# Optimization experiments

Measured on AMD Instinct MI355X. Metric: run time of the kernel, lower is better.

Reference implementation:

```python
import jax, jax.numpy as jnp
import numpy as np

N = 200000
D = 256          # d_node
H = 1024         # n_hidden
OUT = 4002       # n_out
L = 2001
G = 4096         # number of graphs (static)


def _linear_params(key, fan_in, fan_out):
    kw, kb = jax.random.split(key)
    s = 1.0 / np.sqrt(fan_in)
    W = jax.random.uniform(kw, (fan_in, fan_out), jnp.float32, -s, s)
    b = jax.random.uniform(kb, (fan_out,), jnp.float32, -s, s)
    return W, b


def setup_inputs() -> dict:
    key = jax.random.key(0)
    ks = jax.random.split(key, 6)
    h = jax.random.normal(ks[0], (N, D), dtype=jnp.float32)
    node_graph_index = jnp.sort(jax.random.randint(ks[1], (N,), 0, G, dtype=jnp.int32))
    W_pool, b_pool = _linear_params(ks[2], D, D)
    W1, b1 = _linear_params(ks[3], D, H)
    W2, b2 = _linear_params(ks[4], H, H)
    W3, b3 = _linear_params(ks[5], H, OUT)
    return {"h": h, "node_graph_index": node_graph_index,
            "W_pool": W_pool, "b_pool": b_pool,
            "W1": W1, "b1": b1, "W2": W2, "b2": b2, "W3": W3, "b3": b3}


def reference(h, node_graph_index, W_pool, b_pool, W1, b1, W2, b2, W3, b3):
    # attention logits per node: SiLU(W_pool h + b)   [N, D]
    att = jax.nn.silu(h @ W_pool + b_pool)
    # per-graph, per-feature softmax over nodes (segment softmax)
    att_max = jax.ops.segment_max(att, node_graph_index, num_segments=G)   # [G, D]
    att_exp = jnp.exp(att - att_max[node_graph_index])                     # [N, D]
    att_sum = jax.ops.segment_sum(att_exp, node_graph_index, num_segments=G)  # [G, D]
    att_norm = att_exp / jnp.maximum(att_sum[node_graph_index], 1e-12)     # [N, D]
    # attention-weighted pooling
    h_G = jax.ops.segment_sum(h * att_norm, node_graph_index, num_segments=G)  # [G, D]
    # output MLP (depth=2 hidden SiLU layers, plain last)
    x = jax.nn.silu(h_G @ W1 + b1)
    x = jax.nn.silu(x @ W2 + b2)
    out = x @ W3 + b3                                                      # [G, 4002]
    eps_imag = out[:, :L]
    eps_real = out[:, L:]
    return out, eps_imag, eps_real
```

## Files before the change

### kernel.cpp

```cpp
#include <hip/hip_runtime.h>
#include <cstdint>
#include <cstddef>

#define NN 200000
#define DD 256
#define HH 1024
#define OUTD 4002
#define LL 2001
#define GG 4096

#define ROWS_PB 128
#define STEPS 8
#define SLOTS_L 8
#define SLOTS_G 4

typedef unsigned short u16;
typedef short short8 __attribute__((ext_vector_type(8)));
typedef float f32x4 __attribute__((ext_vector_type(4)));

static __device__ __forceinline__ u16 f2bf(float f) {
  uint32_t u = __float_as_uint(f);
  uint32_t r = (u + 0x7FFFu + ((u >> 16) & 1u)) >> 16;
  return (u16)r;
}
static __device__ __forceinline__ float bf2f(u16 b) {
  return __uint_as_float(((uint32_t)b) << 16);
}

static __device__ __forceinline__ void gld_lds16(const void* g, void* l) {
  __builtin_amdgcn_global_load_lds((const __attribute__((address_space(1))) void*)g,
                                   (__attribute__((address_space(3))) void*)l,
                                   16, 0, 0);
}

static __device__ __forceinline__ void barrier_nodrain() {
  asm volatile("s_waitcnt lgkmcnt(0)" ::: "memory");
  __builtin_amdgcn_s_barrier();
  __builtin_amdgcn_sched_barrier(0);
}

__global__ __launch_bounds__(256) void transpose_bf16(const float* __restrict__ W,
                                                      u16* __restrict__ WT,
                                                      int K, int Nc) {
  __shared__ float tile[32][33];
  int nt = blockIdx.x * 32, kt = blockIdx.y * 32;
  int tx = threadIdx.x & 31, ty = threadIdx.x >> 5;
#pragma unroll
  for (int i = 0; i < 4; ++i) {
    int k = kt + ty + i * 8, n = nt + tx;
    tile[ty + i * 8][tx] = (k < K && n < Nc) ? W[(size_t)k * Nc + n] : 0.f;
  }
  __syncthreads();
#pragma unroll
  for (int i = 0; i < 4; ++i) {
    int n = nt + ty + i * 8, k = kt + tx;
    if (n < Nc && k < K) WT[(size_t)n * K + k] = f2bf(tile[tx][ty + i * 8]);
  }
}

__global__ void graph_offsets(const int* __restrict__ idx, int* __restrict__ offs) {
  int g = blockIdx.x * blockDim.x + threadIdx.x;
  if (g > GG) return;
  int lo = 0, hi = NN;
  while (lo < hi) {
    int mid = (lo + hi) >> 1;
    if (idx[mid] < g) lo = mid + 1; else hi = mid;
  }
  offs[g] = lo;
}

__global__ __launch_bounds__(512) void fused_pool(const float* __restrict__ h,
                                                  const u16* __restrict__ WT,
                                                  const float* __restrict__ bias,
                                                  const int* __restrict__ idx,
                                                  const int* __restrict__ offs,
                                                  float* __restrict__ PS_ss,
                                                  float* __restrict__ PS_ah) {
  __shared__ __align__(16) u16 At[2][16 * 256];
  __shared__ float accS[SLOTS_L * 256];
  __shared__ float accA[SLOTS_L * 256];
  __shared__ int lidx[ROWS_PB];

  const int tid = threadIdx.x;
  const int wave = tid >> 6, lane = tid & 63;
  const int rl = lane & 15, q = lane >> 4;
  const int b = blockIdx.x;
  const long row0 = (long)b * ROWS_PB;

  if (tid < ROWS_PB) {
    long r = row0 + tid;
    lidx[tid] = (r < NN) ? idx[r] : -1;
  }
  for (int i = tid; i < SLOTS_L * 256; i += 512) { accS[i] = 0.f; accA[i] = 0.f; }

  const int f0 = wave * 32 + rl, f1 = f0 + 16;
  short8 Bf0[8], Bf1[8];
  {
    const u16* wp0 = WT + (size_t)f0 * 256 + q * 8;
    const u16* wp1 = WT + (size_t)f1 * 256 + q * 8;
#pragma unroll
    for (int k0 = 0; k0 < 8; ++k0) {
      Bf0[k0] = *reinterpret_cast<const short8*>(wp0 + k0 * 32);
      Bf1[k0] = *reinterpret_cast<const short8*>(wp1 + k0 * 32);
    }
  }
  const float bv0 = bias[f0], bv1 = bias[f1];

  const int tr = tid >> 5, te = (tid & 31) * 8;
  const int wbyte = tr * 512 + ((te * 2) ^ ((tr & 7) << 4));
  float4 pf0, pf1;
  auto issue = [&](int st) {
    long r = row0 + (long)st * 16 + tr;
    if (r >= NN) r = NN - 1;
    const float* p = h + r * 256 + te;
    pf0 = *reinterpret_cast<const float4*>(p);
    pf1 = *reinterpret_cast<const float4*>(p + 4);
  };
  auto commit = [&](int bufsel) {
    short8 w;
    w[0] = (short)f2bf(pf0.x); w[1] = (short)f2bf(pf0.y);
    w[2] = (short)f2bf(pf0.z); w[3] = (short)f2bf(pf0.w);
    w[4] = (short)f2bf(pf1.x); w[5] = (short)f2bf(pf1.y);
    w[6] = (short)f2bf(pf1.z); w[7] = (short)f2bf(pf1.w);
    *reinterpret_cast<short8*>((char*)&At[0][0] + bufsel * 8192 + wbyte) = w;
  };

  int afoff[8], hv0off[4], hv1off[4];
#pragma unroll
  for (int k0 = 0; k0 < 8; ++k0)
    afoff[k0] = rl * 512 + ((k0 * 64 + q * 16) ^ ((rl & 7) << 4));
#pragma unroll
  for (int reg = 0; reg < 4; ++reg) {
    int rloc = q * 4 + reg;
    hv0off[reg] = rloc * 512 + ((f0 * 2) ^ ((rloc & 7) << 4));
    hv1off[reg] = rloc * 512 + ((f1 * 2) ^ ((rloc & 7) << 4));
  }

  issue(0);
  commit(0);
  issue(1);
  barrier_nodrain();

  const int gfirst = lidx[0];
  int cur = -1;
  float ss0 = 0.f, ss1 = 0.f, ah0 = 0.f, ah1 = 0.f;

#pragma unroll
  for (int st = 0; st < STEPS; ++st) {
    const char* Ab = (const char*)&At[0][0] + (st & 1) * 8192;
    short8 af[8];
#pragma unroll
    for (int k0 = 0; k0 < 8; ++k0)
      af[k0] = *reinterpret_cast<const short8*>(Ab + afoff[k0]);
    f32x4 acc0 = {0.f, 0.f, 0.f, 0.f}, acc1 = {0.f, 0.f, 0.f, 0.f};
#pragma unroll
    for (int k0 = 0; k0 < 8; ++k0) {
      acc0 = __builtin_amdgcn_mfma_f32_16x16x32_bf16(af[k0], Bf0[k0], acc0, 0, 0, 0);
      acc1 = __builtin_amdgcn_mfma_f32_16x16x32_bf16(af[k0], Bf1[k0], acc1, 0, 0, 0);
    }
#pragma unroll
    for (int reg = 0; reg < 4; ++reg) {
      const int rloc = q * 4 + reg;
      const int gid = lidx[st * 16 + rloc];
      float z0 = acc0[reg] + bv0, z1 = acc1[reg] + bv1;
      float a0 = z0 / (1.f + __expf(-z0));
      float a1 = z1 / (1.f + __expf(-z1));
      float x0 = __expf(a0), x1 = __expf(a1);
      float hv0 = bf2f(*reinterpret_cast<const u16*>(Ab + hv0off[reg]));
      float hv1 = bf2f(*reinterpret_cast<const u16*>(Ab + hv1off[reg]));
      if (gid != cur) {
        if (cur >= 0) {
          int sl = cur - gfirst; if (sl >= SLOTS_L) sl = SLOTS_L - 1;
          atomicAdd(&accS[sl * 256 + f0], ss0);
          atomicAdd(&accA[sl * 256 + f0], ah0);
          atomicAdd(&accS[sl * 256 + f1], ss1);
          atomicAdd(&accA[sl * 256 + f1], ah1);
        }
        ss0 = ss1 = ah0 = ah1 = 0.f;
        cur = gid;
      }
      if (gid >= 0) {
        ss0 += x0; ah0 = __builtin_fmaf(x0, hv0, ah0);
        ss1 += x1; ah1 = __builtin_fmaf(x1, hv1, ah1);
      }
    }
    if (st + 1 < STEPS) {
      commit((st + 1) & 1);
      if (st + 2 < STEPS) issue(st + 2);
    }
    barrier_nodrain();
  }

  if (cur >= 0) {
    int sl = cur - gfirst; if (sl >= SLOTS_L) sl = SLOTS_L - 1;
    atomicAdd(&accS[sl * 256 + f0], ss0);
    atomicAdd(&accA[sl * 256 + f0], ah0);
    atomicAdd(&accS[sl * 256 + f1], ss1);
    atomicAdd(&accA[sl * 256 + f1], ah1);
  }
  __syncthreads();

  long lastrow = row0 + ROWS_PB - 1; if (lastrow >= NN) lastrow = NN - 1;
  const int glast = idx[lastrow];
  int gspan = glast - gfirst + 1; if (gspan > SLOTS_L) gspan = SLOTS_L;
  const int f = tid & 255, which = tid >> 8;
  for (int s = 0; s < gspan; ++s) {
    int g = gfirst + s;
    int osl = b - (offs[g] >> 7);
    if (osl < 0) osl = 0;
    if (osl >= SLOTS_G) osl = SLOTS_G - 1;
    float v = which ? accA[s * 256 + f] : accS[s * 256 + f];
    float* dst = which ? PS_ah : PS_ss;
    dst[((size_t)g * SLOTS_G + osl) * 256 + f] = v;
  }
}

__global__ __launch_bounds__(256) void finalize_pool(const float* __restrict__ PS_ss,
                                                     const float* __restrict__ PS_ah,
                                                     const int* __restrict__ offs,
                                                     u16* __restrict__ hG) {
  int i = blockIdx.x * 256 + threadIdx.x;
  int g = i >> 8, f = i & 255;
  int s0 = offs[g], s1 = offs[g + 1];
  float o = 0.f;
  if (s1 > s0) {
    int b0 = s0 >> 7, b1 = (s1 - 1) >> 7;
    int nsl = b1 - b0 + 1; if (nsl > SLOTS_G) nsl = SLOTS_G;
    float ss = 0.f, ah = 0.f;
    for (int s = 0; s < nsl; ++s) {
      ss += PS_ss[((size_t)g * SLOTS_G + s) * 256 + f];
      ah += PS_ah[((size_t)g * SLOTS_G + s) * 256 + f];
    }
    o = ah / fmaxf(ss, 1e-12f);
  }
  hG[i] = f2bf(o);
}

template <int SILU, int MODE, int BK>
__global__ __launch_bounds__(512) void gemm_bt(const u16* __restrict__ A,
                                               const u16* __restrict__ BT,
                                               const float* __restrict__ bias,
                                               u16* __restrict__ Cb,
                                               float* __restrict__ Cf,
                                               float* __restrict__ Ci,
                                               float* __restrict__ Cr,
                                               int M, int Nn, int K) {
  constexpr int NSUB = BK / 32;
  __shared__ __align__(16) u16 As[2][NSUB][128 * 32];
  __shared__ __align__(16) u16 Bs[2][NSUB][128 * 32];
  const int tid = threadIdx.x;
  const int wave = tid >> 6, lane = tid & 63;
  const int wr = wave >> 2, wc = wave & 3;
  const long bm = (long)blockIdx.y * 128;
  const long bn = (long)blockIdx.x * 128;

  const f32x4 zero = {0.f, 0.f, 0.f, 0.f};
  f32x4 acc[4][2];
#pragma unroll
  for (int i = 0; i < 4; ++i)
#pragma unroll
    for (int j = 0; j < 2; ++j) acc[i][j] = zero;

  const int rg = lane >> 2;
  const int kc = (lane & 3) * 8;
  const int rl = lane & 15;
  const int kk = (lane >> 4) * 8;
  const int rbase = wave * 16;
  const int nt = K / BK;

  auto stage = [&](int t, int buf) {
    const long k0 = (long)t * BK;
#pragma unroll
    for (int s = 0; s < NSUB; ++s) {
      long rA = bm + rbase + rg; if (rA >= M) rA = M - 1;
      long rB = bn + rbase + rg; if (rB >= Nn) rB = Nn - 1;
      gld_lds16(A + rA * K + k0 + s * 32 + kc, &As[buf][s][rbase * 32]);
      gld_lds16(BT + rB * K + k0 + s * 32 + kc, &Bs[buf][s][rbase * 32]);
    }
  };

  stage(0, 0);
  for (int t = 0; t < nt; ++t) {
    const int buf = t & 1;
    if (t + 1 < nt) {
      stage(t + 1, buf ^ 1);
      if constexpr (NSUB == 1) {
        asm volatile("s_waitcnt vmcnt(2)" ::: "memory");
      } else {
        asm volatile("s_waitcnt vmcnt(4)" ::: "memory");
      }
    } else {
      asm volatile("s_waitcnt vmcnt(0)" ::: "memory");
    }
    __builtin_amdgcn_s_barrier();
    __builtin_amdgcn_sched_barrier(0);

#pragma unroll
    for (int s = 0; s < NSUB; ++s) {
      short8 af[4], bfr[2];
#pragma unroll
      for (int mi = 0; mi < 4; ++mi)
        af[mi] = *reinterpret_cast<const short8*>(&As[buf][s][(wr * 64 + mi * 16 + rl) * 32 + kk]);
#pragma unroll
      for (int ni = 0; ni < 2; ++ni)
        bfr[ni] = *reinterpret_cast<const short8*>(&Bs[buf][s][(wc * 32 + ni * 16 + rl) * 32 + kk]);
#pragma unroll
      for (int mi = 0; mi < 4; ++mi)
#pragma unroll
        for (int ni = 0; ni < 2; ++ni)
          acc[mi][ni] = __builtin_amdgcn_mfma_f32_16x16x32_bf16(af[mi], bfr[ni], acc[mi][ni], 0, 0, 0);
    }

    asm volatile("s_waitcnt lgkmcnt(0)" ::: "memory");
    __builtin_amdgcn_s_barrier();
    __builtin_amdgcn_sched_barrier(0);
  }

#pragma unroll
  for (int ni = 0; ni < 2; ++ni) {
    long ccol = bn + wc * 32 + ni * 16 + rl;
    if (ccol >= Nn) continue;
    float bv = bias[ccol];
#pragma unroll
    for (int mi = 0; mi < 4; ++mi) {
#pragma unroll
      for (int reg = 0; reg < 4; ++reg) {
        long rrow = bm + wr * 64 + mi * 16 + (lane >> 4) * 4 + reg;
        if (rrow >= M) continue;
        float v = acc[mi][ni][reg] + bv;
        if (SILU) v = v / (1.f + __expf(-v));
        if (MODE == 0) {
          Cb[rrow * Nn + ccol] = f2bf(v);
        } else {
          Cf[rrow * (long)OUTD + ccol] = v;
          if (ccol < LL) Ci[rrow * (long)LL + ccol] = v;
          else           Cr[rrow * (long)LL + (ccol - LL)] = v;
        }
      }
    }
  }
}

extern "C" void kernel_launch(void* const* d_in, const int* in_sizes, int n_in,
                              void* d_out, int out_size, void* d_ws, size_t ws_size,
                              hipStream_t stream) {
  const float* h      = (const float*)d_in[0];
  const int*   idx    = (const int*)d_in[1];
  const float* W_pool = (const float*)d_in[2];
  const float* b_pool = (const float*)d_in[3];
  const float* W1     = (const float*)d_in[4];
  const float* b1     = (const float*)d_in[5];
  const float* W2     = (const float*)d_in[6];
  const float* b2     = (const float*)d_in[7];
  const float* W3     = (const float*)d_in[8];
  const float* b3     = (const float*)d_in[9];

  float* out   = (float*)d_out;
  float* out_i = out + (size_t)GG * OUTD;
  float* out_r = out_i + (size_t)GG * LL;

  char* ws = (char*)d_ws;
  size_t off = 0;
  auto alloc = [&](size_t bytes) {
    void* p = ws + off;
    off += (bytes + 255) & ~(size_t)255;
    return p;
  };
  u16* WpoolT = (u16*)alloc((size_t)DD * DD * 2);
  u16* W1T    = (u16*)alloc((size_t)HH * DD * 2);
  u16* W2T    = (u16*)alloc((size_t)HH * HH * 2);
  u16* W3T    = (u16*)alloc((size_t)OUTD * HH * 2);
  u16* hG     = (u16*)alloc((size_t)GG * DD * 2);
  u16* x1     = (u16*)alloc((size_t)GG * HH * 2);
  u16* x2     = (u16*)alloc((size_t)GG * HH * 2);
  int* offs   = (int*)alloc((GG + 1) * sizeof(int));
  float* PS_ss = (float*)alloc((size_t)GG * SLOTS_G * 256 * 4);
  float* PS_ah = (float*)alloc((size_t)GG * SLOTS_G * 256 * 4);

  transpose_bf16<<<dim3(8, 8), 256, 0, stream>>>(W_pool, WpoolT, DD, DD);
  transpose_bf16<<<dim3(32, 8), 256, 0, stream>>>(W1, W1T, DD, HH);
  transpose_bf16<<<dim3(32, 32), 256, 0, stream>>>(W2, W2T, HH, HH);
  transpose_bf16<<<dim3(126, 32), 256, 0, stream>>>(W3, W3T, HH, OUTD);
  graph_offsets<<<(GG + 256) / 256, 256, 0, stream>>>(idx, offs);

  fused_pool<<<(NN + ROWS_PB - 1) / ROWS_PB, 512, 0, stream>>>(
      h, WpoolT, b_pool, idx, offs, PS_ss, PS_ah);
  finalize_pool<<<GG, 256, 0, stream>>>(PS_ss, PS_ah, offs, hG);

  gemm_bt<1, 0, 64><<<dim3(8, 32), 512, 0, stream>>>(
      hG, W1T, b1, x1, nullptr, nullptr, nullptr, GG, HH, DD);
  gemm_bt<1, 0, 64><<<dim3(8, 32), 512, 0, stream>>>(
      x1, W2T, b2, x2, nullptr, nullptr, nullptr, GG, HH, HH);
  gemm_bt<0, 1, 32><<<dim3(32, 32), 512, 0, stream>>>(
      x2, W3T, b3, nullptr, out, out_i, out_r, GG, OUTD, HH);
}
```

Before: 287.0 us.

## Split pooling kernel across two feature halves per row chunk

The fused pooling kernel now launches a 2D grid in which each block handles 128 of the 256 output features for its 128-row chunk, instead of all 256. Each wave computes one MFMA output tile instead of two, which halves per-thread registers and LDS accumulators and doubles the number of blocks, aiming at higher occupancy and parallelism. In exchange, every h row chunk is loaded and converted to bf16 twice, once by each half-block, which doubles global reads of the largest input and the conversion work.

```diff
diff --git a/kernel.cpp b/kernel.cpp
--- a/kernel.cpp
+++ b/kernel.cpp
@@ -77,34 +77,34 @@
                                                   float* __restrict__ PS_ss,
                                                   float* __restrict__ PS_ah) {
   __shared__ __align__(16) u16 At[2][16 * 256];
-  __shared__ float accS[SLOTS_L * 256];
-  __shared__ float accA[SLOTS_L * 256];
+  __shared__ float accS[SLOTS_L * 128];
+  __shared__ float accA[SLOTS_L * 128];
   __shared__ int lidx[ROWS_PB];
 
   const int tid = threadIdx.x;
   const int wave = tid >> 6, lane = tid & 63;
   const int rl = lane & 15, q = lane >> 4;
-  const int b = blockIdx.x;
-  const long row0 = (long)b * ROWS_PB;
+  const int half = blockIdx.x;
+  const int chunk = blockIdx.y;
+  const int halfbase = half * 128;
+  const long row0 = (long)chunk * ROWS_PB;
 
   if (tid < ROWS_PB) {
     long r = row0 + tid;
     lidx[tid] = (r < NN) ? idx[r] : -1;
   }
-  for (int i = tid; i < SLOTS_L * 256; i += 512) { accS[i] = 0.f; accA[i] = 0.f; }
-
-  const int f0 = wave * 32 + rl, f1 = f0 + 16;
-  short8 Bf0[8], Bf1[8];
+  for (int i = tid; i < SLOTS_L * 128; i += 512) { accS[i] = 0.f; accA[i] = 0.f; }
+
+  const int fl = wave * 16 + rl;
+  const int f0 = halfbase + fl;
+  short8 Bf0[8];
   {
     const u16* wp0 = WT + (size_t)f0 * 256 + q * 8;
-    const u16* wp1 = WT + (size_t)f1 * 256 + q * 8;
-#pragma unroll
-    for (int k0 = 0; k0 < 8; ++k0) {
+#pragma unroll
+    for (int k0 = 0; k0 < 8; ++k0)
       Bf0[k0] = *reinterpret_cast<const short8*>(wp0 + k0 * 32);
-      Bf1[k0] = *reinterpret_cast<const short8*>(wp1 + k0 * 32);
-    }
-  }
-  const float bv0 = bias[f0], bv1 = bias[f1];
+  }
+  const float bv0 = bias[f0];
 
   const int tr = tid >> 5, te = (tid & 31) * 8;
   const int wbyte = tr * 512 + ((te * 2) ^ ((tr & 7) << 4));
@@ -125,7 +125,7 @@
     *reinterpret_cast<short8*>((char*)&At[0][0] + bufsel * 8192 + wbyte) = w;
   };
 
-  int afoff[8], hv0off[4], hv1off[4];
+  int afoff[8], hv0off[4];
 #pragma unroll
   for (int k0 = 0; k0 < 8; ++k0)
     afoff[k0] = rl * 512 + ((k0 * 64 + q * 16) ^ ((rl & 7) << 4));
@@ -133,7 +133,6 @@
   for (int reg = 0; reg < 4; ++reg) {
     int rloc = q * 4 + reg;
     hv0off[reg] = rloc * 512 + ((f0 * 2) ^ ((rloc & 7) << 4));
-    hv1off[reg] = rloc * 512 + ((f1 * 2) ^ ((rloc & 7) << 4));
   }
 
   issue(0);
@@ -143,7 +142,7 @@
 
   const int gfirst = lidx[0];
   int cur = -1;
-  float ss0 = 0.f, ss1 = 0.f, ah0 = 0.f, ah1 = 0.f;
+  float ss0 = 0.f, ah0 = 0.f;
 
 #pragma unroll
   for (int st = 0; st < STEPS; ++st) {
@@ -152,36 +151,30 @@
 #pragma unroll
     for (int k0 = 0; k0 < 8; ++k0)
       af[k0] = *reinterpret_cast<const short8*>(Ab + afoff[k0]);
-    f32x4 acc0 = {0.f, 0.f, 0.f, 0.f}, acc1 = {0.f, 0.f, 0.f, 0.f};
-#pragma unroll
-    for (int k0 = 0; k0 < 8; ++k0) {
+    f32x4 acc0 = {0.f, 0.f, 0.f, 0.f};
+#pragma unroll
+    for (int k0 = 0; k0 < 8; ++k0)
       acc0 = __builtin_amdgcn_mfma_f32_16x16x32_bf16(af[k0], Bf0[k0], acc0, 0, 0, 0);
-      acc1 = __builtin_amdgcn_mfma_f32_16x16x32_bf16(af[k0], Bf1[k0], acc1, 0, 0, 0);
-    }
 #pragma unroll
     for (int reg = 0; reg < 4; ++reg) {
       const int rloc = q * 4 + reg;
       const int gid = lidx[st * 16 + rloc];
-      float z0 = acc0[reg] + bv0, z1 = acc1[reg] + bv1;
+      float z0 = acc0[reg] + bv0;
       float a0 = z0 / (1.f + __expf(-z0));
-      float a1 = z1 / (1.f + __expf(-z1));
-      float x0 = __expf(a0), x1 = __expf(a1);
+      float x0 = __expf(a0);
       float hv0 = bf2f(*reinterpret_cast<const u16*>(Ab + hv0off[reg]));
-      float hv1 = bf2f(*reinterpret_cast<const u16*>(Ab + hv1off[reg]));
       if (gid != cur) {
         if (cur >= 0) {
           int sl = cur - gfirst; if (sl >= SLOTS_L) sl = SLOTS_L - 1;
-          atomicAdd(&accS[sl * 256 + f0], ss0);
-          atomicAdd(&accA[sl * 256 + f0], ah0);
-          atomicAdd(&accS[sl * 256 + f1], ss1);
-          atomicAdd(&accA[sl * 256 + f1], ah1);
+          atomicAdd(&accS[sl * 128 + fl], ss0);
+          atomicAdd(&accA[sl * 128 + fl], ah0);
         }
-        ss0 = ss1 = ah0 = ah1 = 0.f;
+        ss0 = ah0 = 0.f;
         cur = gid;
       }
       if (gid >= 0) {
-        ss0 += x0; ah0 = __builtin_fmaf(x0, hv0, ah0);
-        ss1 += x1; ah1 = __builtin_fmaf(x1, hv1, ah1);
+        ss0 += x0;
+        ah0 = __builtin_fmaf(x0, hv0, ah0);
       }
     }
     if (st + 1 < STEPS) {
@@ -193,25 +186,23 @@
 
   if (cur >= 0) {
     int sl = cur - gfirst; if (sl >= SLOTS_L) sl = SLOTS_L - 1;
-    atomicAdd(&accS[sl * 256 + f0], ss0);
-    atomicAdd(&accA[sl * 256 + f0], ah0);
-    atomicAdd(&accS[sl * 256 + f1], ss1);
-    atomicAdd(&accA[sl * 256 + f1], ah1);
+    atomicAdd(&accS[sl * 128 + fl], ss0);
+    atomicAdd(&accA[sl * 128 + fl], ah0);
   }
   __syncthreads();
 
   long lastrow = row0 + ROWS_PB - 1; if (lastrow >= NN) lastrow = NN - 1;
   const int glast = idx[lastrow];
   int gspan = glast - gfirst + 1; if (gspan > SLOTS_L) gspan = SLOTS_L;
-  const int f = tid & 255, which = tid >> 8;
-  for (int s = 0; s < gspan; ++s) {
+  const int f = tid & 127, which = (tid >> 7) & 1;
+  for (int s = tid >> 8; s < gspan; s += 2) {
     int g = gfirst + s;
-    int osl = b - (offs[g] >> 7);
+    int osl = chunk - (offs[g] >> 7);
     if (osl < 0) osl = 0;
     if (osl >= SLOTS_G) osl = SLOTS_G - 1;
-    float v = which ? accA[s * 256 + f] : accS[s * 256 + f];
+    float v = which ? accA[s * 128 + f] : accS[s * 128 + f];
     float* dst = which ? PS_ah : PS_ss;
-    dst[((size_t)g * SLOTS_G + osl) * 256 + f] = v;
+    dst[((size_t)g * SLOTS_G + osl) * 256 + halfbase + f] = v;
   }
 }
 
@@ -383,7 +374,7 @@
   transpose_bf16<<<dim3(126, 32), 256, 0, stream>>>(W3, W3T, HH, OUTD);
   graph_offsets<<<(GG + 256) / 256, 256, 0, stream>>>(idx, offs);
 
-  fused_pool<<<(NN + ROWS_PB - 1) / ROWS_PB, 512, 0, stream>>>(
+  fused_pool<<<dim3(2, (NN + ROWS_PB - 1) / ROWS_PB), 512, 0, stream>>>(
       h, WpoolT, b_pool, idx, offs, PS_ss, PS_ah);
   finalize_pool<<<GG, 256, 0, stream>>>(PS_ss, PS_ah, offs, hG);
 
```

Result: slower. 309.3 us (+7.8%).

## Stage fp32 h tiles via direct global-to-LDS loads with triple buffering

Applied to the files above, without the earlier changes.

Replaces the register-staged h loads and manual bf16 conversion into LDS with global_load_lds DMA of raw fp32 rows into a 3-deep swizzled LDS ring. Conversion to bf16 now happens after the LDS read using packed cvt instructions, and the pooling h values are read as fp32. The change is meant to cut VGPR staging and conversion work on the load path and to deepen the prefetch. In exchange it doubles LDS footprint per stage and LDS read bandwidth, and it pins occupancy with waves_per_eu.

```diff
diff --git a/kernel.cpp b/kernel.cpp
--- a/kernel.cpp
+++ b/kernel.cpp
@@ -17,14 +17,12 @@
 typedef unsigned short u16;
 typedef short short8 __attribute__((ext_vector_type(8)));
 typedef float f32x4 __attribute__((ext_vector_type(4)));
+typedef unsigned int uint4v __attribute__((ext_vector_type(4)));
 
 static __device__ __forceinline__ u16 f2bf(float f) {
   uint32_t u = __float_as_uint(f);
   uint32_t r = (u + 0x7FFFu + ((u >> 16) & 1u)) >> 16;
   return (u16)r;
-}
-static __device__ __forceinline__ float bf2f(u16 b) {
-  return __uint_as_float(((uint32_t)b) << 16);
 }
 
 static __device__ __forceinline__ void gld_lds16(const void* g, void* l) {
@@ -69,14 +67,15 @@
   offs[g] = lo;
 }
 
-__global__ __launch_bounds__(512) void fused_pool(const float* __restrict__ h,
-                                                  const u16* __restrict__ WT,
-                                                  const float* __restrict__ bias,
-                                                  const int* __restrict__ idx,
-                                                  const int* __restrict__ offs,
-                                                  float* __restrict__ PS_ss,
-                                                  float* __restrict__ PS_ah) {
-  __shared__ __align__(16) u16 At[2][16 * 256];
+__global__ __launch_bounds__(512) __attribute__((amdgpu_waves_per_eu(4, 4)))
+void fused_pool(const float* __restrict__ h,
+                const u16* __restrict__ WT,
+                const float* __restrict__ bias,
+                const int* __restrict__ idx,
+                const int* __restrict__ offs,
+                float* __restrict__ PS_ss,
+                float* __restrict__ PS_ah) {
+  __shared__ __align__(16) float At[3][16 * 256];
   __shared__ float accS[SLOTS_L * 256];
   __shared__ float accA[SLOTS_L * 256];
   __shared__ int lidx[ROWS_PB];
@@ -104,41 +103,28 @@
       Bf1[k0] = *reinterpret_cast<const short8*>(wp1 + k0 * 32);
     }
   }
+  asm volatile("" : "+v"(Bf0[0]), "+v"(Bf0[1]), "+v"(Bf0[2]), "+v"(Bf0[3]),
+                    "+v"(Bf0[4]), "+v"(Bf0[5]), "+v"(Bf0[6]), "+v"(Bf0[7]));
+  asm volatile("" : "+v"(Bf1[0]), "+v"(Bf1[1]), "+v"(Bf1[2]), "+v"(Bf1[3]),
+                    "+v"(Bf1[4]), "+v"(Bf1[5]), "+v"(Bf1[6]), "+v"(Bf1[7]));
   const float bv0 = bias[f0], bv1 = bias[f1];
 
-  const int tr = tid >> 5, te = (tid & 31) * 8;
-  const int wbyte = tr * 512 + ((te * 2) ^ ((tr & 7) << 4));
-  float4 pf0, pf1;
-  auto issue = [&](int st) {
-    long r = row0 + (long)st * 16 + tr;
-    if (r >= NN) r = NN - 1;
-    const float* p = h + r * 256 + te;
-    pf0 = *reinterpret_cast<const float4*>(p);
-    pf1 = *reinterpret_cast<const float4*>(p + 4);
+  const int r_a = wave * 2, r_b = r_a + 1;
+  const int sga = (lane ^ (r_a & 7)) * 4;
+  const int sgb = (lane ^ (r_b & 7)) * 4;
+  auto stage = [&](int st) {
+    int bu = st % 3;
+    long ra = row0 + (long)st * 16 + r_a; if (ra >= NN) ra = NN - 1;
+    long rb = row0 + (long)st * 16 + r_b; if (rb >= NN) rb = NN - 1;
+    gld_lds16(h + ra * 256 + sga, &At[bu][r_a * 256]);
+    gld_lds16(h + rb * 256 + sgb, &At[bu][r_b * 256]);
   };
-  auto commit = [&](int bufsel) {
-    short8 w;
-    w[0] = (short)f2bf(pf0.x); w[1] = (short)f2bf(pf0.y);
-    w[2] = (short)f2bf(pf0.z); w[3] = (short)f2bf(pf0.w);
-    w[4] = (short)f2bf(pf1.x); w[5] = (short)f2bf(pf1.y);
-    w[6] = (short)f2bf(pf1.z); w[7] = (short)f2bf(pf1.w);
-    *reinterpret_cast<short8*>((char*)&At[0][0] + bufsel * 8192 + wbyte) = w;
-  };
-
-  int afoff[8], hv0off[4], hv1off[4];
-#pragma unroll
-  for (int k0 = 0; k0 < 8; ++k0)
-    afoff[k0] = rl * 512 + ((k0 * 64 + q * 16) ^ ((rl & 7) << 4));
-#pragma unroll
-  for (int reg = 0; reg < 4; ++reg) {
-    int rloc = q * 4 + reg;
-    hv0off[reg] = rloc * 512 + ((f0 * 2) ^ ((rloc & 7) << 4));
-    hv1off[reg] = rloc * 512 + ((f1 * 2) ^ ((rloc & 7) << 4));
-  }
-
-  issue(0);
-  commit(0);
-  issue(1);
+
+  const int swz = (rl & 7) << 4;
+
+  stage(0);
+  stage(1);
+  asm volatile("s_waitcnt vmcnt(2)" ::: "memory");
   barrier_nodrain();
 
   const int gfirst = lidx[0];
@@ -147,27 +133,37 @@
 
 #pragma unroll
   for (int st = 0; st < STEPS; ++st) {
-    const char* Ab = (const char*)&At[0][0] + (st & 1) * 8192;
-    short8 af[8];
-#pragma unroll
-    for (int k0 = 0; k0 < 8; ++k0)
-      af[k0] = *reinterpret_cast<const short8*>(Ab + afoff[k0]);
+    const char* Ab = (const char*)&At[st % 3][0];
+    if (st + 2 < STEPS) stage(st + 2);
+
     f32x4 acc0 = {0.f, 0.f, 0.f, 0.f}, acc1 = {0.f, 0.f, 0.f, 0.f};
 #pragma unroll
     for (int k0 = 0; k0 < 8; ++k0) {
-      acc0 = __builtin_amdgcn_mfma_f32_16x16x32_bf16(af[k0], Bf0[k0], acc0, 0, 0, 0);
-      acc1 = __builtin_amdgcn_mfma_f32_16x16x32_bf16(af[k0], Bf1[k0], acc1, 0, 0, 0);
-    }
+      const int o0 = rl * 1024 + ((k0 * 128 + q * 32) ^ swz);
+      f32x4 lo = *reinterpret_cast<const f32x4*>(Ab + o0);
+      f32x4 hi = *reinterpret_cast<const f32x4*>(Ab + (o0 ^ 16));
+      uint32_t p0, p1, p2, p3;
+      asm("v_cvt_pk_bf16_f32 %0, %1, %2" : "=v"(p0) : "v"(lo[0]), "v"(lo[1]));
+      asm("v_cvt_pk_bf16_f32 %0, %1, %2" : "=v"(p1) : "v"(lo[2]), "v"(lo[3]));
+      asm("v_cvt_pk_bf16_f32 %0, %1, %2" : "=v"(p2) : "v"(hi[0]), "v"(hi[1]));
+      asm("v_cvt_pk_bf16_f32 %0, %1, %2" : "=v"(p3) : "v"(hi[2]), "v"(hi[3]));
+      uint4v u = {p0, p1, p2, p3};
+      short8 af = __builtin_bit_cast(short8, u);
+      acc0 = __builtin_amdgcn_mfma_f32_16x16x32_bf16(af, Bf0[k0], acc0, 0, 0, 0);
+      acc1 = __builtin_amdgcn_mfma_f32_16x16x32_bf16(af, Bf1[k0], acc1, 0, 0, 0);
+    }
+
 #pragma unroll
     for (int reg = 0; reg < 4; ++reg) {
       const int rloc = q * 4 + reg;
       const int gid = lidx[st * 16 + rloc];
+      const int rsw = (rloc & 7) << 4;
+      float hv0 = *reinterpret_cast<const float*>(Ab + rloc * 1024 + ((f0 * 4) ^ rsw));
+      float hv1 = *reinterpret_cast<const float*>(Ab + rloc * 1024 + ((f1 * 4) ^ rsw));
       float z0 = acc0[reg] + bv0, z1 = acc1[reg] + bv1;
       float a0 = z0 / (1.f + __expf(-z0));
       float a1 = z1 / (1.f + __expf(-z1));
       float x0 = __expf(a0), x1 = __expf(a1);
-      float hv0 = bf2f(*reinterpret_cast<const u16*>(Ab + hv0off[reg]));
-      float hv1 = bf2f(*reinterpret_cast<const u16*>(Ab + hv1off[reg]));
       if (gid != cur) {
         if (cur >= 0) {
           int sl = cur - gfirst; if (sl >= SLOTS_L) sl = SLOTS_L - 1;
@@ -184,11 +180,14 @@
         ss1 += x1; ah1 = __builtin_fmaf(x1, hv1, ah1);
       }
     }
-    if (st + 1 < STEPS) {
-      commit((st + 1) & 1);
-      if (st + 2 < STEPS) issue(st + 2);
-    }
-    barrier_nodrain();
+
+    if (st + 2 < STEPS) {
+      asm volatile("s_waitcnt vmcnt(2) lgkmcnt(0)" ::: "memory");
+    } else {
+      asm volatile("s_waitcnt vmcnt(0) lgkmcnt(0)" ::: "memory");
+    }
+    __builtin_amdgcn_s_barrier();
+    __builtin_amdgcn_sched_barrier(0);
   }
 
   if (cur >= 0) {
```

Result: slower. 385.4 us (+34.3%).
